# Optimization experiments

Measured on AMD Instinct MI355X. Metric: run time of the kernel, lower is better.

Reference implementation:

```python
import jax, jax.numpy as jnp
import numpy as np

B, N = 4, 20                        # batch, qubits
L = int(np.ceil(np.log2(N)))        # 5 layers, one 4x4 generator each


def setup_inputs():
    key = jax.random.key(0)
    k1, k2, k3, k4 = jax.random.split(key, 4)
    psi_re = jax.random.normal(k1, (B, 2 ** N), dtype=jnp.float32)
    psi_im = jax.random.normal(k2, (B, 2 ** N), dtype=jnp.float32)
    nrm = jnp.sqrt(jnp.sum(psi_re ** 2 + psi_im ** 2, axis=1, keepdims=True))
    psi_re, psi_im = psi_re / nrm, psi_im / nrm   # normalized quantum state
    H_re = jax.random.normal(k3, (L, 4, 4), dtype=jnp.float32)
    H_im = jax.random.normal(k4, (L, 4, 4), dtype=jnp.float32)
    return {"psi_re": psi_re, "psi_im": psi_im, "H_re": H_re, "H_im": H_im}


def _make_unitary(A):
    # torch.matrix_exp(A - A^H): expm of an anti-Hermitian generator via eigh
    G = A - A.conj().T
    w, V = jnp.linalg.eigh(-1j * G)            # G = i * Hermitian
    return (V * jnp.exp(1j * w)) @ V.conj().T  # expm(G), unitary


def _apply_gate(T, U4, axes):
    # contract 4x4 gate (reshaped [2,2,2,2]) onto two qubit axes of tensor T
    T = jnp.tensordot(U4, T, axes=((2, 3), axes))
    return jnp.moveaxis(T, (0, 1), axes)


def _gate_pairs(nq):
    pairs = [(2 * i, 2 * i + 1) for i in range(nq // 2)]
    if nq > 2:
        pairs += [(2 * i + 1, (2 * i + 2) % nq) for i in range(nq // 2)]
    return pairs


def _forward(psi_re, psi_im, H_re, H_im):
    psi = (psi_re + 1j * psi_im).astype(jnp.complex64).reshape((B,) + (2,) * N)
    H = (H_re + 1j * H_im).astype(jnp.complex64)
    state, is_dm, nq = psi, False, N
    for layer in range(L):
        U = _make_unitary(H[layer]).reshape(2, 2, 2, 2)
        Uc = U.conj()
        # _2local_conv: brick pattern of the same 2-qubit gate
        for (a, b) in _gate_pairs(nq):
            state = _apply_gate(state, U, (1 + a, 1 + b))
            if is_dm:  # density matrix: also apply U* on bra axes
                state = _apply_gate(state, Uc, (1 + nq + a, 1 + nq + b))
        # _2local_pool: measuring qubits 0..nq//2-1 with index shifting removes
        # the even-indexed qubits -> partial trace over them
        if nq >= 2:
            traced = [2 * i for i in range(nq // 2)]
            kept = [q for q in range(nq) if q not in traced]
            t, k = len(traced), len(kept)
            if is_dm:
                perm = (0,) + tuple(1 + q for q in kept) + tuple(1 + q for q in traced) \
                     + tuple(1 + nq + q for q in kept) + tuple(1 + nq + q for q in traced)
                r = jnp.transpose(state, perm).reshape(B, 2 ** k, 2 ** t, 2 ** k, 2 ** t)
                state = jnp.einsum('bitjt->bij', r).reshape((B,) + (2,) * k + (2,) * k)
            else:
                perm = (0,) + tuple(1 + q for q in traced) + tuple(1 + q for q in kept)
                p = jnp.transpose(state, perm).reshape(B, 2 ** t, 2 ** k)
                state = jnp.einsum('bti,btj->bij', p, p.conj()).reshape((B,) + (2,) * k + (2,) * k)
                is_dm = True
            nq = k
    # final state.measure(0): reduced 1-qubit density matrix, take P(outcome 0)
    r = state.reshape(B, 2, 2 ** (nq - 1), 2, 2 ** (nq - 1))
    rho0 = jnp.einsum('birjr->bij', r)
    return rho0[:, 0, 0].real


def reference(psi_re, psi_im, H_re, H_im):
    return _forward(psi_re, psi_im, H_re, H_im)
```

## Files before the change

kernel.cpp:

```cpp
#include <hip/hip_runtime.h>
#include <math.h>


__device__ __forceinline__ float2 cmul(float2 a, float2 b) {
  return make_float2(a.x * b.x - a.y * b.y, a.x * b.y + a.y * b.x);
}
__device__ __forceinline__ float2 cmadd(float2 acc, float2 a, float2 b) {
  acc.x = fmaf(a.x, b.x, fmaf(-a.y, b.y, acc.x));
  acc.y = fmaf(a.x, b.y, fmaf(a.y, b.x, acc.y));
  return acc;
}
__device__ __forceinline__ float2 cmaddc(float2 acc, float2 a, float2 b) {
  acc.x = fmaf(a.x, b.x, fmaf(a.y, b.y, acc.x));
  acc.y = fmaf(a.y, b.x, fmaf(-a.x, b.y, acc.y));
  return acc;
}
__device__ __forceinline__ int pad(int e) { return e + (e >> 4); }

__device__ __forceinline__ unsigned spread(unsigned v) {
  v = (v | (v << 8)) & 0x00FF00FFu;
  v = (v | (v << 4)) & 0x0F0F0F0Fu;
  v = (v | (v << 2)) & 0x33333333u;
  v = (v | (v << 1)) & 0x55555555u;
  return v;
}
__device__ __forceinline__ unsigned spread2(unsigned v) { return spread(spread(v)); }
__device__ __forceinline__ int ins(int x, int p) {
  return ((x >> p) << (p + 1)) | (x & ((1 << p) - 1));
}

__device__ __forceinline__ void gate4(float2& v0, float2& v1, float2& v2, float2& v3,
                                      const float2 (&U)[16]) {
  float2 n0 = cmul(U[0], v0);  n0 = cmadd(n0, U[1], v1);  n0 = cmadd(n0, U[2], v2);  n0 = cmadd(n0, U[3], v3);
  float2 n1 = cmul(U[4], v0);  n1 = cmadd(n1, U[5], v1);  n1 = cmadd(n1, U[6], v2);  n1 = cmadd(n1, U[7], v3);
  float2 n2 = cmul(U[8], v0);  n2 = cmadd(n2, U[9], v1);  n2 = cmadd(n2, U[10], v2); n2 = cmadd(n2, U[11], v3);
  float2 n3 = cmul(U[12], v0); n3 = cmadd(n3, U[13], v1); n3 = cmadd(n3, U[14], v2); n3 = cmadd(n3, U[15], v3);
  v0 = n0; v1 = n1; v2 = n2; v3 = n3;
}

template <int NG>
__device__ __forceinline__ void gate16n(float2 (&v)[16], const float2 (&U)[16]) {
#pragma unroll
  for (int g = 0; g < 4; g++)
    gate4(v[g * 4 + 0], v[g * 4 + 1], v[g * 4 + 2], v[g * 4 + 3], U);
#pragma unroll
  for (int lo = 0; lo < 4; lo++)
    gate4(v[lo], v[lo + 4], v[lo + 8], v[lo + 12], U);
  if (NG == 3) {
#pragma unroll
    for (int b3 = 0; b3 < 2; b3++)
#pragma unroll
      for (int b0 = 0; b0 < 2; b0++) {
        int j = b3 * 8 + b0;
        gate4(v[j], v[j + 2], v[j + 4], v[j + 6], U);
      }
  }
}

__device__ __forceinline__ void apply_gate_tile13(float2* t, const float2 (&U)[16],
                                                  int pa, int pb, int tid) {
  int p0 = pa < pb ? pa : pb;
  int p1 = pa < pb ? pb : pa;
  int m0 = (1 << p0) - 1, m1 = (1 << p1) - 1;
  int ia = 1 << pa, ib = 1 << pb;
#pragma unroll
  for (int g = tid; g < 2048; g += 512) {
    int idx = ((g & ~m0) << 1) | (g & m0);
    idx = ((idx & ~m1) << 1) | (idx & m1);
    int e0 = pad(idx), e1 = pad(idx | ib), e2 = pad(idx | ia), e3 = pad(idx | ia | ib);
    float2 v0 = t[e0], v1 = t[e1], v2 = t[e2], v3 = t[e3];
    gate4(v0, v1, v2, v3, U);
    t[e0] = v0; t[e1] = v1; t[e2] = v2; t[e3] = v3;
  }
}

template <int NG>
__device__ __forceinline__ void phase4_l0(float2* t, const float2 (&U)[16],
                                          int p0, int p1, int p2, int p3, int tid) {
  int o0 = 1 << p0, o1 = 1 << p1, o2 = 1 << p2, o3 = 1 << p3;
  int idx = ins(ins(ins(ins(tid, p0), p1), p2), p3);
  float2 v[16];
#pragma unroll
  for (int j = 0; j < 16; j++) {
    int off = ((j & 1) ? o0 : 0) + ((j & 2) ? o1 : 0) + ((j & 4) ? o2 : 0) + ((j & 8) ? o3 : 0);
    v[j] = t[pad(idx + off)];
  }
  gate16n<NG>(v, U);
#pragma unroll
  for (int j = 0; j < 16; j++) {
    int off = ((j & 1) ? o0 : 0) + ((j & 2) ? o1 : 0) + ((j & 4) ? o2 : 0) + ((j & 8) ? o3 : 0);
    t[pad(idx + off)] = v[j];
  }
}

template <int NG>
__device__ __forceinline__ void phase4_pool(float2* w, const float2 (&U)[16],
                                            int a_lo, int a_hi, int c_lo, int c_hi,
                                            int o0, int o1, int o2, int o3, int tid) {
  int uu = tid & 7, ss = (tid >> 3) & 7, t_lo = tid >> 6;
  int u = ins(ins(uu, a_lo), a_hi);
  int s = ins(ins(ss, c_lo), c_hi);
  int base = t_lo * 1120 + s * 35 + u;
  float2 v[16];
#pragma unroll
  for (int j = 0; j < 16; j++) {
    int off = ((j & 1) ? o0 : 0) + ((j & 2) ? o1 : 0) + ((j & 4) ? o2 : 0) + ((j & 8) ? o3 : 0);
    v[j] = w[base + off];
  }
  gate16n<NG>(v, U);
#pragma unroll
  for (int j = 0; j < 16; j++) {
    int off = ((j & 1) ? o0 : 0) + ((j & 2) ? o1 : 0) + ((j & 4) ? o2 : 0) + ((j & 8) ? o3 : 0);
    w[base + off] = v[j];
  }
}

__device__ __forceinline__ void pool_p3(float2* w, const float2 (&U)[16], int tid) {
#pragma unroll
  for (int it = 0; it < 2; it++) {
    int h = tid + it * 512;
    int uu = h & 7, ss = (h >> 3) & 15, t_lo = h >> 7;
    int base = t_lo * 1120 + (ss << 1) * 35 + (uu << 2);
    float2 v[8];
    v[0] = w[base];      v[1] = w[base + 1];
    v[4] = w[base + 2];  v[5] = w[base + 3];
    v[2] = w[base + 35]; v[3] = w[base + 36];
    v[6] = w[base + 37]; v[7] = w[base + 38];
    gate4(v[0], v[1], v[2], v[3], U);
    gate4(v[4], v[5], v[6], v[7], U);
    gate4(v[0], v[2], v[4], v[6], U);
    gate4(v[1], v[3], v[5], v[7], U);
    w[base] = v[0];      w[base + 1] = v[1];
    w[base + 2] = v[4];  w[base + 3] = v[5];
    w[base + 35] = v[2]; w[base + 36] = v[3];
    w[base + 37] = v[6]; w[base + 38] = v[7];
  }
}

__device__ __forceinline__ float2 expm16(const float* __restrict__ Hre,
                                         const float* __restrict__ Him,
                                         int l, int l16) {
  int r = l16 >> 2, c = l16 & 3;
  double tr = (double)Hre[l * 16 + r * 4 + c] - (double)Hre[l * 16 + c * 4 + r];
  double ti = (double)Him[l * 16 + r * 4 + c] + (double)Him[l * 16 + c * 4 + r];
  double a = sqrt(tr * tr + ti * ti);
  a += __shfl_xor(a, 1, 16);
  a += __shfl_xor(a, 2, 16);
  double nrm = fmax(a, __shfl_xor(a, 4, 16));
  nrm = fmax(nrm, __shfl_xor(nrm, 8, 16));
  int s = 0;
  while (nrm > 0.25 && s < 60) { nrm *= 0.5; s++; }
  double sc = ldexp(1.0, -s);
  tr *= sc; ti *= sc;
  double id = (r == c) ? 1.0 : 0.0;
  double er = id, ei = 0.0, pr = id, pi = 0.0;
  for (int k = 1; k <= 16; k++) {
    double qr = 0.0, qi = 0.0;
#pragma unroll
    for (int m = 0; m < 4; m++) {
      double pmr = __shfl(pr, r * 4 + m, 16);
      double pmi = __shfl(pi, r * 4 + m, 16);
      double tmr = __shfl(tr, m * 4 + c, 16);
      double tmi = __shfl(ti, m * 4 + c, 16);
      qr = fma(pmr, tmr, fma(-pmi, tmi, qr));
      qi = fma(pmr, tmi, fma(pmi, tmr, qi));
    }
    double inv = 1.0 / (double)k;
    pr = qr * inv; pi = qi * inv;
    er += pr; ei += pi;
  }
  for (int it = 0; it < s; it++) {
    double qr = 0.0, qi = 0.0;
#pragma unroll
    for (int m = 0; m < 4; m++) {
      double amr = __shfl(er, r * 4 + m, 16);
      double ami = __shfl(ei, r * 4 + m, 16);
      double bmr = __shfl(er, m * 4 + c, 16);
      double bmi = __shfl(ei, m * 4 + c, 16);
      qr = fma(amr, bmr, fma(-ami, bmi, qr));
      qi = fma(amr, bmi, fma(ami, bmr, qi));
    }
    er = qr; ei = qi;
  }
  return make_float2((float)er, (float)ei);
}

__global__ __launch_bounds__(512, 4) void l0_pass1(const float* __restrict__ pre,
                                                   const float* __restrict__ pim,
                                                   const float* __restrict__ Hre,
                                                   const float* __restrict__ Him,
                                                   float2* __restrict__ Umat,
                                                   float2* __restrict__ state) {
  extern __shared__ float2 tile[];
  __shared__ float2 Ush[16];
  int tid = threadIdx.x;
  int bid = blockIdx.x;
  int b = bid >> 7, hi = bid & 127;
  size_t base = ((size_t)b << 20) | ((size_t)hi << 13);
  for (int e4 = tid; e4 < 2048; e4 += 512) {
    int e = e4 << 2;
    float4 re = *(const float4*)&pre[base + e];
    float4 im = *(const float4*)&pim[base + e];
    int d = pad(e);
    tile[d] = make_float2(re.x, im.x);
    tile[d + 1] = make_float2(re.y, im.y);
    tile[d + 2] = make_float2(re.z, im.z);
    tile[d + 3] = make_float2(re.w, im.w);
  }
  {
    int wv = tid >> 6, g16 = (tid & 63) >> 4, l16 = tid & 15;
    int layer = (wv == 0) ? g16 : ((wv == 1 && g16 == 0) ? 4 : -1);
    if (layer == 0 || (bid == 0 && layer > 0)) {
      float2 ue = expm16(Hre, Him, layer, l16);
      if (layer == 0) Ush[l16] = ue;
      if (bid == 0) Umat[layer * 16 + l16] = ue;
    }
  }
  __syncthreads();
  float2 U[16];
#pragma unroll
  for (int k = 0; k < 16; k++) U[k] = Ush[k];
  phase4_l0<3>(tile, U, 0, 1, 2, 3, tid);   __syncthreads();
  phase4_l0<3>(tile, U, 4, 5, 6, 7, tid);   __syncthreads();
  phase4_l0<3>(tile, U, 8, 9, 10, 11, tid); __syncthreads();
  phase4_l0<2>(tile, U, 3, 4, 7, 8, tid);   __syncthreads();
  for (int e4 = tid; e4 < 2048; e4 += 512) {
    int e = e4 << 2;
    int d = pad(e);
    float2 a = tile[d], b2 = tile[d + 1], c = tile[d + 2], d2 = tile[d + 3];
    float4* dst = (float4*)&state[base + e];
    dst[0] = make_float4(a.x, a.y, b2.x, b2.y);
    dst[1] = make_float4(c.x, c.y, d2.x, d2.y);
  }
}

__global__ __launch_bounds__(512, 4) void l0_pass2(const float2* __restrict__ Umat,
                                                   float2* __restrict__ state) {
  extern __shared__ float2 tile[];
  int tid = threadIdx.x;
  int bid = blockIdx.x;
  int b = bid >> 7, mid = bid & 127;
  size_t base = ((size_t)b << 20) | ((size_t)mid << 4);
  float2 U[16];
#pragma unroll
  for (int k = 0; k < 16; k++) U[k] = Umat[k];
  for (int f = tid; f < 2048; f += 512) {
    int chunk = f >> 2, q = (f & 3) << 2;
    size_t a = base + ((size_t)chunk << 11) + q;
    const float4* src = (const float4*)&state[a];
    float4 v0 = src[0], v1 = src[1];
    int d = pad(chunk * 16 + q);
    tile[d] = make_float2(v0.x, v0.y);
    tile[d + 1] = make_float2(v0.z, v0.w);
    tile[d + 2] = make_float2(v1.x, v1.y);
    tile[d + 3] = make_float2(v1.z, v1.w);
  }
  __syncthreads();
  phase4_l0<3>(tile, U, 5, 6, 7, 8, tid);    __syncthreads();
  phase4_l0<3>(tile, U, 9, 10, 11, 12, tid); __syncthreads();
  phase4_l0<2>(tile, U, 4, 5, 8, 9, tid);    __syncthreads();
  apply_gate_tile13(tile, U, 0, 12, tid);    __syncthreads();
  for (int f = tid; f < 2048; f += 512) {
    int chunk = f >> 2, q = (f & 3) << 2;
    size_t a = base + ((size_t)chunk << 11) + q;
    int d = pad(chunk * 16 + q);
    float2 x0 = tile[d], x1 = tile[d + 1], x2 = tile[d + 2], x3 = tile[d + 3];
    float4* dst = (float4*)&state[a];
    dst[0] = make_float4(x0.x, x0.y, x1.x, x1.y);
    dst[1] = make_float4(x2.x, x2.y, x3.x, x3.y);
  }
}

__global__ __launch_bounds__(512, 4) void pool_l1(const float2* __restrict__ Umat,
                                                  const float2* __restrict__ state,
                                                  float2* __restrict__ partial) {
  extern __shared__ float2 w[];
  int tid = threadIdx.x;
  int bid = blockIdx.x;
  int b = bid >> 7, thi = bid & 127;
  size_t bbase = (size_t)b << 20;
  float2 U[16];
#pragma unroll
  for (int k = 0; k < 16; k++) U[k] = Umat[16 + k];
  unsigned tbase = spread((unsigned)(thi << 3)) << 1;
  for (int f = tid; f < 4096; f += 512) {
    int up = f & 15, s = (f >> 4) & 31, t_lo = f >> 9;
    unsigned addr = tbase | (spread((unsigned)t_lo) << 1) | (spread2((unsigned)up) << 4)
                  | (spread2((unsigned)s) << 2);
    float4 v = *(const float4*)&state[bbase + (size_t)addr];
    int c = t_lo * 1120 + s * 35 + (up << 1);
    w[c] = make_float2(v.x, v.y);
    w[c + 1] = make_float2(v.z, v.w);
  }
  __syncthreads();
  phase4_pool<3>(w, U, 3, 4, 3, 4, 8, 280, 16, 560, tid); __syncthreads();
  phase4_pool<3>(w, U, 1, 2, 1, 2, 2, 70, 4, 140, tid);   __syncthreads();
  pool_p3(w, U, tid);                                     __syncthreads();
  phase4_pool<2>(w, U, 0, 3, 2, 4, 140, 8, 560, 1, tid);  __syncthreads();
  int wv = tid >> 6, lane = tid & 63;
  int u0 = (lane >> 3) << 2, v0 = (lane & 7) << 2;
  float2 acc[4][4];
#pragma unroll
  for (int i = 0; i < 4; i++)
#pragma unroll
    for (int j = 0; j < 4; j++) acc[i][j] = make_float2(0.f, 0.f);
  {
    int tb = wv * 1120;
#pragma unroll 4
    for (int s = 0; s < 32; s++) {
      int row = tb + s * 35;
      float2 x[4], y[4];
#pragma unroll
      for (int i = 0; i < 4; i++) { x[i] = w[row + u0 + i]; y[i] = w[row + v0 + i]; }
#pragma unroll
      for (int i = 0; i < 4; i++)
#pragma unroll
        for (int j = 0; j < 4; j++) acc[i][j] = cmaddc(acc[i][j], x[i], y[j]);
    }
  }
  __syncthreads();
  if (wv > 0) {
#pragma unroll
    for (int i = 0; i < 4; i++)
#pragma unroll
      for (int j = 0; j < 4; j++)
        w[(wv - 1) * 1024 + (u0 + i) * 32 + (v0 + j)] = acc[i][j];
  }
  __syncthreads();
  if (wv == 0) {
    float2* outp = partial + ((size_t)bid << 10);
#pragma unroll
    for (int i = 0; i < 4; i++)
#pragma unroll
      for (int j = 0; j < 4; j++) {
        float2 a = acc[i][j];
#pragma unroll
        for (int k = 0; k < 7; k++) {
          float2 o = w[k * 1024 + (u0 + i) * 32 + (v0 + j)];
          a.x += o.x; a.y += o.y;
        }
        outp[(u0 + i) * 32 + (v0 + j)] = a;
      }
  }
}

__global__ __launch_bounds__(256) void reduce_partials(const float4* __restrict__ partial,
                                                       float4* __restrict__ rho32) {
  int gid = blockIdx.x * 256 + threadIdx.x;
  int b = gid >> 9, p = gid & 511;
  float4 acc = make_float4(0.f, 0.f, 0.f, 0.f);
#pragma unroll 4
  for (int h = 0; h < 128; h++) {
    float4 v = partial[(((b << 7) + h) << 9) + p];
    acc.x += v.x; acc.y += v.y; acc.z += v.z; acc.w += v.w;
  }
  rho32[gid] = acc;
}

__global__ __launch_bounds__(256) void finish(const float2* __restrict__ Umat,
                                              const float2* __restrict__ rho32,
                                              float* __restrict__ out) {
  __shared__ float2 rho[1024];
  __shared__ float2 r3s[64];
  __shared__ float2 r4s[16];
  int tid = threadIdx.x;
  int b = blockIdx.x;
  for (int p = tid; p < 1024; p += 256) rho[p] = rho32[(b << 10) + p];
  __syncthreads();

  float2 U[16], Uc[16];
#pragma unroll
  for (int k = 0; k < 16; k++) { U[k] = Umat[32 + k]; Uc[k] = make_float2(U[k].x, -U[k].y); }
  const int gl2[4][2] = {{4,3},{2,1},{3,2},{1,0}};
#pragma unroll
  for (int gi = 0; gi < 4; gi++) {
    int pa = gl2[gi][0], pb = gl2[gi][1];
    int p0 = pa < pb ? pa : pb, p1 = pa < pb ? pb : pa;
    int m0 = (1 << p0) - 1, m1 = (1 << p1) - 1;
    int ia = 1 << pa, ib = 1 << pb;
    {
      int j = tid >> 3, g = tid & 7;
      int idx = ((g & ~m0) << 1) | (g & m0);
      idx = ((idx & ~m1) << 1) | (idx & m1);
      float2 v0 = rho[idx * 32 + j], v1 = rho[(idx | ib) * 32 + j];
      float2 v2 = rho[(idx | ia) * 32 + j], v3 = rho[(idx | ia | ib) * 32 + j];
      gate4(v0, v1, v2, v3, U);
      rho[idx * 32 + j] = v0; rho[(idx | ib) * 32 + j] = v1;
      rho[(idx | ia) * 32 + j] = v2; rho[(idx | ia | ib) * 32 + j] = v3;
    }
    __syncthreads();
    {
      int i = tid >> 3, g = tid & 7;
      int idx = ((g & ~m0) << 1) | (g & m0);
      idx = ((idx & ~m1) << 1) | (idx & m1);
      float2 v0 = rho[i * 32 + idx], v1 = rho[i * 32 + (idx | ib)];
      float2 v2 = rho[i * 32 + (idx | ia)], v3 = rho[i * 32 + (idx | ia | ib)];
      gate4(v0, v1, v2, v3, Uc);
      rho[i * 32 + idx] = v0; rho[i * 32 + (idx | ib)] = v1;
      rho[i * 32 + (idx | ia)] = v2; rho[i * 32 + (idx | ia | ib)] = v3;
    }
    __syncthreads();
  }
  if (tid < 64) {
    int u = tid >> 3, v = tid & 7;
    float2 acc = {0.f, 0.f};
#pragma unroll
    for (int s = 0; s < 4; s++) {
      int iu = ((s >> 1) << 4) | ((u >> 2) << 3) | ((s & 1) << 2) | (((u >> 1) & 1) << 1) | (u & 1);
      int iv = ((s >> 1) << 4) | ((v >> 2) << 3) | ((s & 1) << 2) | (((v >> 1) & 1) << 1) | (v & 1);
      float2 x = rho[iu * 32 + iv];
      acc.x += x.x; acc.y += x.y;
    }
    r3s[u * 8 + v] = acc;
  }
  __syncthreads();

#pragma unroll
  for (int k = 0; k < 16; k++) { U[k] = Umat[48 + k]; Uc[k] = make_float2(U[k].x, -U[k].y); }
  const int gl3[2][2] = {{2,1},{1,0}};
#pragma unroll
  for (int gi = 0; gi < 2; gi++) {
    int pa = gl3[gi][0], pb = gl3[gi][1];
    int p0 = pa < pb ? pa : pb, p1 = pa < pb ? pb : pa;
    int m0 = (1 << p0) - 1, m1 = (1 << p1) - 1;
    int ia = 1 << pa, ib = 1 << pb;
    if (tid < 16) {
      int j = tid >> 1, g = tid & 1;
      int idx = ((g & ~m0) << 1) | (g & m0);
      idx = ((idx & ~m1) << 1) | (idx & m1);
      float2 v0 = r3s[idx * 8 + j], v1 = r3s[(idx | ib) * 8 + j];
      float2 v2 = r3s[(idx | ia) * 8 + j], v3 = r3s[(idx | ia | ib) * 8 + j];
      gate4(v0, v1, v2, v3, U);
      r3s[idx * 8 + j] = v0; r3s[(idx | ib) * 8 + j] = v1;
      r3s[(idx | ia) * 8 + j] = v2; r3s[(idx | ia | ib) * 8 + j] = v3;
    }
    __syncthreads();
    if (tid < 16) {
      int i = tid >> 1, g = tid & 1;
      int idx = ((g & ~m0) << 1) | (g & m0);
      idx = ((idx & ~m1) << 1) | (idx & m1);
      float2 v0 = r3s[i * 8 + idx], v1 = r3s[i * 8 + (idx | ib)];
      float2 v2 = r3s[i * 8 + (idx | ia)], v3 = r3s[i * 8 + (idx | ia | ib)];
      gate4(v0, v1, v2, v3, Uc);
      r3s[i * 8 + idx] = v0; r3s[i * 8 + (idx | ib)] = v1;
      r3s[i * 8 + (idx | ia)] = v2; r3s[i * 8 + (idx | ia | ib)] = v3;
    }
    __syncthreads();
  }
  if (tid < 16) {
    int u = tid >> 2, v = tid & 3;
    float2 acc = {0.f, 0.f};
#pragma unroll
    for (int s = 0; s < 2; s++) {
      float2 x = r3s[((s << 2) | u) * 8 + ((s << 2) | v)];
      acc.x += x.x; acc.y += x.y;
    }
    r4s[u * 4 + v] = acc;
  }
  __syncthreads();

#pragma unroll
  for (int k = 0; k < 16; k++) { U[k] = Umat[64 + k]; Uc[k] = make_float2(U[k].x, -U[k].y); }
  if (tid < 4) {
    int j = tid;
    float2 v0 = r4s[0 * 4 + j], v1 = r4s[1 * 4 + j], v2 = r4s[2 * 4 + j], v3 = r4s[3 * 4 + j];
    gate4(v0, v1, v2, v3, U);
    r4s[0 * 4 + j] = v0; r4s[1 * 4 + j] = v1; r4s[2 * 4 + j] = v2; r4s[3 * 4 + j] = v3;
  }
  __syncthreads();
  if (tid < 4) {
    int i = tid;
    float2 v0 = r4s[i * 4 + 0], v1 = r4s[i * 4 + 1], v2 = r4s[i * 4 + 2], v3 = r4s[i * 4 + 3];
    gate4(v0, v1, v2, v3, Uc);
    r4s[i * 4 + 0] = v0; r4s[i * 4 + 1] = v1; r4s[i * 4 + 2] = v2; r4s[i * 4 + 3] = v3;
  }
  __syncthreads();
  if (tid == 0) out[b] = r4s[0].x + r4s[10].x;
}

extern "C" void kernel_launch(void* const* d_in, const int* in_sizes, int n_in,
                              void* d_out, int out_size, void* d_ws, size_t ws_size,
                              hipStream_t stream) {
  const float* psi_re = (const float*)d_in[0];
  const float* psi_im = (const float*)d_in[1];
  const float* H_re = (const float*)d_in[2];
  const float* H_im = (const float*)d_in[3];
  float* out = (float*)d_out;

  char* ws = (char*)d_ws;
  float2* Umat = (float2*)ws;
  float2* state = (float2*)(ws + 4096);
  float* partial = (float*)(ws + 4096 + ((size_t)1 << 25));
  float* rho32 = (float*)(ws + 4096 + ((size_t)1 << 25) + ((size_t)1 << 22));

  const size_t LDS_L0 = 8704 * sizeof(float2);
  const size_t LDS_POOL = 8960 * sizeof(float2);

  hipLaunchKernelGGL(l0_pass1, dim3(512), dim3(512), LDS_L0, stream,
                     psi_re, psi_im, H_re, H_im, Umat, state);
  hipLaunchKernelGGL(l0_pass2, dim3(512), dim3(512), LDS_L0, stream,
                     (const float2*)Umat, state);
  hipLaunchKernelGGL(pool_l1, dim3(512), dim3(512), LDS_POOL, stream,
                     (const float2*)Umat, (const float2*)state, (float2*)partial);
  hipLaunchKernelGGL(reduce_partials, dim3(8), dim3(256), 0, stream,
                     (const float4*)partial, (float4*)rho32);
  hipLaunchKernelGGL(finish, dim3(4), dim3(256), 0, stream,
                     (const float2*)Umat, (const float2*)rho32, out);
}
```

Measured before the change: 183.9 us.

## Halve tile sizes and block width; split pool_l1 into two streamed chunks

The layer-0 passes now use 4096-element tiles (12 qubits) with 256-thread blocks and twice as many blocks. The gate placement is reshuffled to match: pass1 handles qubits 0-11 and pass2 handles qubits 11-19 plus the 0/11 pair. pool_l1 runs 256 threads and processes its 8 t-slices in two chunks of 4 through half-size LDS, accumulating the density-matrix product across chunks. The aim is lower LDS use per block and more resident blocks for better occupancy and latency hiding. The cost is more synchronisation, more strided global accesses in pass2, and a different gate partition that must still cover every pair.

```diff
diff --git a/kernel.cpp b/kernel.cpp
--- a/kernel.cpp
+++ b/kernel.cpp
@@ -57,14 +57,14 @@
   }
 }
 
-__device__ __forceinline__ void apply_gate_tile13(float2* t, const float2 (&U)[16],
+__device__ __forceinline__ void apply_gate_tile12(float2* t, const float2 (&U)[16],
                                                   int pa, int pb, int tid) {
   int p0 = pa < pb ? pa : pb;
   int p1 = pa < pb ? pb : pa;
   int m0 = (1 << p0) - 1, m1 = (1 << p1) - 1;
   int ia = 1 << pa, ib = 1 << pb;
 #pragma unroll
-  for (int g = tid; g < 2048; g += 512) {
+  for (int g = tid; g < 1024; g += 256) {
     int idx = ((g & ~m0) << 1) | (g & m0);
     idx = ((idx & ~m1) << 1) | (idx & m1);
     int e0 = pad(idx), e1 = pad(idx | ib), e2 = pad(idx | ia), e3 = pad(idx | ia | ib);
@@ -118,7 +118,7 @@
 __device__ __forceinline__ void pool_p3(float2* w, const float2 (&U)[16], int tid) {
 #pragma unroll
   for (int it = 0; it < 2; it++) {
-    int h = tid + it * 512;
+    int h = tid + it * 256;
     int uu = h & 7, ss = (h >> 3) & 15, t_lo = h >> 7;
     int base = t_lo * 1120 + (ss << 1) * 35 + (uu << 2);
     float2 v[8];
@@ -185,7 +185,7 @@
   return make_float2((float)er, (float)ei);
 }
 
-__global__ __launch_bounds__(512, 4) void l0_pass1(const float* __restrict__ pre,
+__global__ __launch_bounds__(256, 4) void l0_pass1(const float* __restrict__ pre,
                                                    const float* __restrict__ pim,
                                                    const float* __restrict__ Hre,
                                                    const float* __restrict__ Him,
@@ -195,10 +195,10 @@
   __shared__ float2 Ush[16];
   int tid = threadIdx.x;
   int bid = blockIdx.x;
-  int b = bid >> 7, hi = bid & 127;
-  size_t base = ((size_t)b << 20) | ((size_t)hi << 13);
-  for (int e4 = tid; e4 < 2048; e4 += 512) {
-    int e = e4 << 2;
+  int b = bid >> 8, hi = bid & 255;
+  size_t base = ((size_t)b << 20) | ((size_t)hi << 12);
+  for (int f = tid; f < 1024; f += 256) {
+    int e = f << 2;
     float4 re = *(const float4*)&pre[base + e];
     float4 im = *(const float4*)&pim[base + e];
     int d = pad(e);
@@ -224,8 +224,8 @@
   phase4_l0<3>(tile, U, 4, 5, 6, 7, tid);   __syncthreads();
   phase4_l0<3>(tile, U, 8, 9, 10, 11, tid); __syncthreads();
   phase4_l0<2>(tile, U, 3, 4, 7, 8, tid);   __syncthreads();
-  for (int e4 = tid; e4 < 2048; e4 += 512) {
-    int e = e4 << 2;
+  for (int f = tid; f < 1024; f += 256) {
+    int e = f << 2;
     int d = pad(e);
     float2 a = tile[d], b2 = tile[d + 1], c = tile[d + 2], d2 = tile[d + 3];
     float4* dst = (float4*)&state[base + e];
@@ -234,44 +234,45 @@
   }
 }
 
-__global__ __launch_bounds__(512, 4) void l0_pass2(const float2* __restrict__ Umat,
+__global__ __launch_bounds__(256, 4) void l0_pass2(const float2* __restrict__ Umat,
                                                    float2* __restrict__ state) {
   extern __shared__ float2 tile[];
   int tid = threadIdx.x;
   int bid = blockIdx.x;
-  int b = bid >> 7, mid = bid & 127;
-  size_t base = ((size_t)b << 20) | ((size_t)mid << 4);
+  int b = bid >> 8, mid = bid & 255;
+  size_t base = ((size_t)b << 20) | ((size_t)mid << 3);
   float2 U[16];
 #pragma unroll
   for (int k = 0; k < 16; k++) U[k] = Umat[k];
-  for (int f = tid; f < 2048; f += 512) {
-    int chunk = f >> 2, q = (f & 3) << 2;
-    size_t a = base + ((size_t)chunk << 11) + q;
+  for (int c = tid; c < 512; c += 256) {
+    size_t a = base + ((size_t)c << 11);
     const float4* src = (const float4*)&state[a];
-    float4 v0 = src[0], v1 = src[1];
-    int d = pad(chunk * 16 + q);
-    tile[d] = make_float2(v0.x, v0.y);
-    tile[d + 1] = make_float2(v0.z, v0.w);
-    tile[d + 2] = make_float2(v1.x, v1.y);
-    tile[d + 3] = make_float2(v1.z, v1.w);
-  }
-  __syncthreads();
-  phase4_l0<3>(tile, U, 5, 6, 7, 8, tid);    __syncthreads();
-  phase4_l0<3>(tile, U, 9, 10, 11, 12, tid); __syncthreads();
-  phase4_l0<2>(tile, U, 4, 5, 8, 9, tid);    __syncthreads();
-  apply_gate_tile13(tile, U, 0, 12, tid);    __syncthreads();
-  for (int f = tid; f < 2048; f += 512) {
-    int chunk = f >> 2, q = (f & 3) << 2;
-    size_t a = base + ((size_t)chunk << 11) + q;
-    int d = pad(chunk * 16 + q);
-    float2 x0 = tile[d], x1 = tile[d + 1], x2 = tile[d + 2], x3 = tile[d + 3];
+    int d = pad(c * 8);
+#pragma unroll
+    for (int q = 0; q < 4; q++) {
+      float4 v = src[q];
+      tile[d + 2 * q] = make_float2(v.x, v.y);
+      tile[d + 2 * q + 1] = make_float2(v.z, v.w);
+    }
+  }
+  __syncthreads();
+  phase4_l0<3>(tile, U, 4, 5, 6, 7, tid);   __syncthreads();
+  phase4_l0<3>(tile, U, 8, 9, 10, 11, tid); __syncthreads();
+  phase4_l0<2>(tile, U, 3, 4, 7, 8, tid);   __syncthreads();
+  apply_gate_tile12(tile, U, 0, 11, tid);   __syncthreads();
+  for (int c = tid; c < 512; c += 256) {
+    size_t a = base + ((size_t)c << 11);
     float4* dst = (float4*)&state[a];
-    dst[0] = make_float4(x0.x, x0.y, x1.x, x1.y);
-    dst[1] = make_float4(x2.x, x2.y, x3.x, x3.y);
-  }
-}
-
-__global__ __launch_bounds__(512, 4) void pool_l1(const float2* __restrict__ Umat,
+    int d = pad(c * 8);
+#pragma unroll
+    for (int q = 0; q < 4; q++) {
+      float2 x0 = tile[d + 2 * q], x1 = tile[d + 2 * q + 1];
+      dst[q] = make_float4(x0.x, x0.y, x1.x, x1.y);
+    }
+  }
+}
+
+__global__ __launch_bounds__(256, 4) void pool_l1(const float2* __restrict__ Umat,
                                                   const float2* __restrict__ state,
                                                   float2* __restrict__ partial) {
   extern __shared__ float2 w[];
@@ -283,20 +284,7 @@
 #pragma unroll
   for (int k = 0; k < 16; k++) U[k] = Umat[16 + k];
   unsigned tbase = spread((unsigned)(thi << 3)) << 1;
-  for (int f = tid; f < 4096; f += 512) {
-    int up = f & 15, s = (f >> 4) & 31, t_lo = f >> 9;
-    unsigned addr = tbase | (spread((unsigned)t_lo) << 1) | (spread2((unsigned)up) << 4)
-                  | (spread2((unsigned)s) << 2);
-    float4 v = *(const float4*)&state[bbase + (size_t)addr];
-    int c = t_lo * 1120 + s * 35 + (up << 1);
-    w[c] = make_float2(v.x, v.y);
-    w[c + 1] = make_float2(v.z, v.w);
-  }
-  __syncthreads();
-  phase4_pool<3>(w, U, 3, 4, 3, 4, 8, 280, 16, 560, tid); __syncthreads();
-  phase4_pool<3>(w, U, 1, 2, 1, 2, 2, 70, 4, 140, tid);   __syncthreads();
-  pool_p3(w, U, tid);                                     __syncthreads();
-  phase4_pool<2>(w, U, 0, 3, 2, 4, 140, 8, 560, 1, tid);  __syncthreads();
+
   int wv = tid >> 6, lane = tid & 63;
   int u0 = (lane >> 3) << 2, v0 = (lane & 7) << 2;
   float2 acc[4][4];
@@ -304,18 +292,37 @@
   for (int i = 0; i < 4; i++)
 #pragma unroll
     for (int j = 0; j < 4; j++) acc[i][j] = make_float2(0.f, 0.f);
-  {
-    int tb = wv * 1120;
+
+  for (int chunk = 0; chunk < 2; chunk++) {
+    if (chunk) __syncthreads();
+    for (int f = tid; f < 2048; f += 256) {
+      int up = f & 15, s = (f >> 4) & 31, tl = f >> 9;
+      int t3 = chunk * 4 + tl;
+      unsigned addr = tbase | (spread((unsigned)t3) << 1) | (spread2((unsigned)up) << 4)
+                    | (spread2((unsigned)s) << 2);
+      float4 v = *(const float4*)&state[bbase + (size_t)addr];
+      int c = tl * 1120 + s * 35 + (up << 1);
+      w[c] = make_float2(v.x, v.y);
+      w[c + 1] = make_float2(v.z, v.w);
+    }
+    __syncthreads();
+    phase4_pool<3>(w, U, 3, 4, 3, 4, 8, 280, 16, 560, tid); __syncthreads();
+    phase4_pool<3>(w, U, 1, 2, 1, 2, 2, 70, 4, 140, tid);   __syncthreads();
+    pool_p3(w, U, tid);                                     __syncthreads();
+    phase4_pool<2>(w, U, 0, 3, 2, 4, 140, 8, 560, 1, tid);  __syncthreads();
+    {
+      int tb = wv * 1120;
 #pragma unroll 4
-    for (int s = 0; s < 32; s++) {
-      int row = tb + s * 35;
-      float2 x[4], y[4];
-#pragma unroll
-      for (int i = 0; i < 4; i++) { x[i] = w[row + u0 + i]; y[i] = w[row + v0 + i]; }
-#pragma unroll
-      for (int i = 0; i < 4; i++)
-#pragma unroll
-        for (int j = 0; j < 4; j++) acc[i][j] = cmaddc(acc[i][j], x[i], y[j]);
+      for (int s = 0; s < 32; s++) {
+        int row = tb + s * 35;
+        float2 x[4], y[4];
+#pragma unroll
+        for (int i = 0; i < 4; i++) { x[i] = w[row + u0 + i]; y[i] = w[row + v0 + i]; }
+#pragma unroll
+        for (int i = 0; i < 4; i++)
+#pragma unroll
+          for (int j = 0; j < 4; j++) acc[i][j] = cmaddc(acc[i][j], x[i], y[j]);
+      }
     }
   }
   __syncthreads();
@@ -335,7 +342,7 @@
       for (int j = 0; j < 4; j++) {
         float2 a = acc[i][j];
 #pragma unroll
-        for (int k = 0; k < 7; k++) {
+        for (int k = 0; k < 3; k++) {
           float2 o = w[k * 1024 + (u0 + i) * 32 + (v0 + j)];
           a.x += o.x; a.y += o.y;
         }
@@ -493,14 +500,14 @@
   float* partial = (float*)(ws + 4096 + ((size_t)1 << 25));
   float* rho32 = (float*)(ws + 4096 + ((size_t)1 << 25) + ((size_t)1 << 22));
 
-  const size_t LDS_L0 = 8704 * sizeof(float2);
-  const size_t LDS_POOL = 8960 * sizeof(float2);
-
-  hipLaunchKernelGGL(l0_pass1, dim3(512), dim3(512), LDS_L0, stream,
+  const size_t LDS_L0 = 4352 * sizeof(float2);
+  const size_t LDS_POOL = 4480 * sizeof(float2);
+
+  hipLaunchKernelGGL(l0_pass1, dim3(1024), dim3(256), LDS_L0, stream,
                      psi_re, psi_im, H_re, H_im, Umat, state);
-  hipLaunchKernelGGL(l0_pass2, dim3(512), dim3(512), LDS_L0, stream,
+  hipLaunchKernelGGL(l0_pass2, dim3(1024), dim3(256), LDS_L0, stream,
                      (const float2*)Umat, state);
-  hipLaunchKernelGGL(pool_l1, dim3(512), dim3(512), LDS_POOL, stream,
+  hipLaunchKernelGGL(pool_l1, dim3(512), dim3(256), LDS_POOL, stream,
                      (const float2*)Umat, (const float2*)state, (float2*)partial);
   hipLaunchKernelGGL(reduce_partials, dim3(8), dim3(256), 0, stream,
                      (const float4*)partial, (float4*)rho32);
```

New measurement: 193.1 us. +5.0%, slower.

## Permute intermediate state layout so pool_l1 reads contiguous blocks

Applied to the files above, without the earlier changes.

Changes the global memory layout of the intermediate state written by the first layer-0 kernel to a bit-permuted order. The second layer-0 pass and the pooling kernel now read it as contiguous runs instead of strided or bit-spread gathers. Gate qubit positions and offsets are remapped accordingly through a generalized phase4 helper. This aims to improve coalescing of the pool_l1 loads, in exchange for scattered float4 stores in the first pass and more complex index bookkeeping.

```diff
diff --git a/kernel.cpp b/kernel.cpp
--- a/kernel.cpp
+++ b/kernel.cpp
@@ -16,15 +16,6 @@
   return acc;
 }
 __device__ __forceinline__ int pad(int e) { return e + (e >> 4); }
-
-__device__ __forceinline__ unsigned spread(unsigned v) {
-  v = (v | (v << 8)) & 0x00FF00FFu;
-  v = (v | (v << 4)) & 0x0F0F0F0Fu;
-  v = (v | (v << 2)) & 0x33333333u;
-  v = (v | (v << 1)) & 0x55555555u;
-  return v;
-}
-__device__ __forceinline__ unsigned spread2(unsigned v) { return spread(spread(v)); }
 __device__ __forceinline__ int ins(int x, int p) {
   return ((x >> p) << (p + 1)) | (x & ((1 << p) - 1));
 }
@@ -75,10 +66,10 @@
 }
 
 template <int NG>
-__device__ __forceinline__ void phase4_l0(float2* t, const float2 (&U)[16],
-                                          int p0, int p1, int p2, int p3, int tid) {
-  int o0 = 1 << p0, o1 = 1 << p1, o2 = 1 << p2, o3 = 1 << p3;
-  int idx = ins(ins(ins(ins(tid, p0), p1), p2), p3);
+__device__ __forceinline__ void phase4_f(float2* t, const float2 (&U)[16],
+                                         int q0, int q1, int q2, int q3,
+                                         int o0, int o1, int o2, int o3, int tid) {
+  int idx = ins(ins(ins(ins(tid, q0), q1), q2), q3);
   float2 v[16];
 #pragma unroll
   for (int j = 0; j < 16; j++) {
@@ -220,17 +211,25 @@
   float2 U[16];
 #pragma unroll
   for (int k = 0; k < 16; k++) U[k] = Ush[k];
-  phase4_l0<3>(tile, U, 0, 1, 2, 3, tid);   __syncthreads();
-  phase4_l0<3>(tile, U, 4, 5, 6, 7, tid);   __syncthreads();
-  phase4_l0<3>(tile, U, 8, 9, 10, 11, tid); __syncthreads();
-  phase4_l0<2>(tile, U, 3, 4, 7, 8, tid);   __syncthreads();
+  phase4_f<3>(tile, U, 0, 1, 2, 3, 1, 2, 4, 8, tid);            __syncthreads();
+  phase4_f<3>(tile, U, 4, 5, 6, 7, 16, 32, 64, 128, tid);       __syncthreads();
+  phase4_f<3>(tile, U, 8, 9, 10, 11, 256, 512, 1024, 2048, tid);__syncthreads();
+  phase4_f<2>(tile, U, 3, 4, 7, 8, 8, 16, 128, 256, tid);       __syncthreads();
+  int hifix = ((hi & 1) << 16) | (((hi >> 1) & 1) << 6) | (((hi >> 2) & 1) << 17)
+            | (((hi >> 3) & 1) << 5) | (((hi >> 4) & 1) << 18) | (((hi >> 5) & 1) << 7)
+            | (((hi >> 6) & 1) << 19);
+  size_t dbase = ((size_t)b << 20) | (unsigned)hifix;
   for (int e4 = tid; e4 < 2048; e4 += 512) {
-    int e = e4 << 2;
-    int d = pad(e);
-    float2 a = tile[d], b2 = tile[d + 1], c = tile[d + 2], d2 = tile[d + 3];
-    float4* dst = (float4*)&state[base + e];
-    dst[0] = make_float4(a.x, a.y, b2.x, b2.y);
-    dst[1] = make_float4(c.x, c.y, d2.x, d2.y);
+    int le = e4;
+    int d = ((le & 1) << 2) | (((le >> 1) & 1) << 3) | (((le >> 2) & 1) << 8)
+          | (((le >> 3) & 1) << 12) | (((le >> 4) & 1) << 10) | (((le >> 5) & 1) << 13)
+          | (((le >> 6) & 1) << 9) | (((le >> 7) & 1) << 14) | (((le >> 8) & 1) << 11)
+          | (((le >> 9) & 1) << 15) | (((le >> 10) & 1) << 4);
+    int src = pad(e4 << 2);
+    float2 x0 = tile[src], x1 = tile[src + 1], x2 = tile[src + 2], x3 = tile[src + 3];
+    float4* dst = (float4*)&state[dbase + d];
+    dst[0] = make_float4(x0.x, x0.y, x1.x, x1.y);
+    dst[1] = make_float4(x2.x, x2.y, x3.x, x3.y);
   }
 }
 
@@ -240,34 +239,29 @@
   int tid = threadIdx.x;
   int bid = blockIdx.x;
   int b = bid >> 7, mid = bid & 127;
-  size_t base = ((size_t)b << 20) | ((size_t)mid << 4);
+  size_t base = ((size_t)b << 20) | ((size_t)mid << 8);
   float2 U[16];
 #pragma unroll
   for (int k = 0; k < 16; k++) U[k] = Umat[k];
-  for (int f = tid; f < 2048; f += 512) {
-    int chunk = f >> 2, q = (f & 3) << 2;
-    size_t a = base + ((size_t)chunk << 11) + q;
-    const float4* src = (const float4*)&state[a];
-    float4 v0 = src[0], v1 = src[1];
-    int d = pad(chunk * 16 + q);
-    tile[d] = make_float2(v0.x, v0.y);
-    tile[d + 1] = make_float2(v0.z, v0.w);
-    tile[d + 2] = make_float2(v1.x, v1.y);
-    tile[d + 3] = make_float2(v1.z, v1.w);
-  }
-  __syncthreads();
-  phase4_l0<3>(tile, U, 5, 6, 7, 8, tid);    __syncthreads();
-  phase4_l0<3>(tile, U, 9, 10, 11, 12, tid); __syncthreads();
-  phase4_l0<2>(tile, U, 4, 5, 8, 9, tid);    __syncthreads();
-  apply_gate_tile13(tile, U, 0, 12, tid);    __syncthreads();
-  for (int f = tid; f < 2048; f += 512) {
-    int chunk = f >> 2, q = (f & 3) << 2;
-    size_t a = base + ((size_t)chunk << 11) + q;
-    int d = pad(chunk * 16 + q);
-    float2 x0 = tile[d], x1 = tile[d + 1], x2 = tile[d + 2], x3 = tile[d + 3];
-    float4* dst = (float4*)&state[a];
-    dst[0] = make_float4(x0.x, x0.y, x1.x, x1.y);
-    dst[1] = make_float4(x2.x, x2.y, x3.x, x3.y);
+  for (int f = tid; f < 4096; f += 512) {
+    int run = f >> 7, idx = f & 127;
+    size_t a = base + ((size_t)run << 15) + ((size_t)idx << 1);
+    float4 v = *(const float4*)&state[a];
+    int d = pad(run * 256 + idx * 2);
+    tile[d] = make_float2(v.x, v.y);
+    tile[d + 1] = make_float2(v.z, v.w);
+  }
+  __syncthreads();
+  phase4_f<3>(tile, U, 4, 6, 9, 10, 16, 512, 64, 1024, tid);    __syncthreads();
+  phase4_f<3>(tile, U, 5, 7, 11, 12, 32, 2048, 128, 4096, tid); __syncthreads();
+  phase4_f<2>(tile, U, 4, 5, 8, 10, 256, 16, 1024, 32, tid);    __syncthreads();
+  apply_gate_tile13(tile, U, 0, 12, tid);                       __syncthreads();
+  for (int f = tid; f < 4096; f += 512) {
+    int run = f >> 7, idx = f & 127;
+    size_t a = base + ((size_t)run << 15) + ((size_t)idx << 1);
+    int d = pad(run * 256 + idx * 2);
+    float2 x0 = tile[d], x1 = tile[d + 1];
+    *(float4*)&state[a] = make_float4(x0.x, x0.y, x1.x, x1.y);
   }
 }
 
@@ -278,17 +272,18 @@
   int tid = threadIdx.x;
   int bid = blockIdx.x;
   int b = bid >> 7, thi = bid & 127;
-  size_t bbase = (size_t)b << 20;
+  size_t base = ((size_t)b << 20) | ((size_t)thi << 13);
   float2 U[16];
 #pragma unroll
   for (int k = 0; k < 16; k++) U[k] = Umat[16 + k];
-  unsigned tbase = spread((unsigned)(thi << 3)) << 1;
   for (int f = tid; f < 4096; f += 512) {
-    int up = f & 15, s = (f >> 4) & 31, t_lo = f >> 9;
-    unsigned addr = tbase | (spread((unsigned)t_lo) << 1) | (spread2((unsigned)up) << 4)
-                  | (spread2((unsigned)s) << 2);
-    float4 v = *(const float4*)&state[bbase + (size_t)addr];
-    int c = t_lo * 1120 + s * 35 + (up << 1);
+    int e = f << 1;
+    float4 v = *(const float4*)&state[base + e];
+    int u = (((e >> 8) & 1) << 1) | (((e >> 9) & 1) << 2) | (((e >> 4) & 1) << 3) | (((e >> 5) & 1) << 4);
+    int s = ((e >> 2) & 1) | (((e >> 10) & 1) << 1) | (((e >> 11) & 1) << 2)
+          | (((e >> 6) & 1) << 3) | (((e >> 7) & 1) << 4);
+    int t = ((e >> 1) & 1) | (((e >> 3) & 1) << 1) | (((e >> 12) & 1) << 2);
+    int c = t * 1120 + s * 35 + u;
     w[c] = make_float2(v.x, v.y);
     w[c + 1] = make_float2(v.z, v.w);
   }
```

Measured after the change: 182.3 us. No clear change (-0.8%).
